# Kernel optimization log

Measured on AMD Instinct MI355X. Metric: run time of the kernel, lower is better.

Reference implementation:

```python
import jax, jax.numpy as jnp
import numpy as np

ALPHA = 0.2          # LeakyReLU negative slope
NEG_BIG = -9e15      # mask fill value from the original code
N, IN_F, OUT_F = 8192, 128, 64


def setup_inputs() -> dict:
    key = jax.random.key(0)
    k1, k2, k3, k4 = jax.random.split(key, 4)
    h = jax.random.normal(k1, (N, IN_F), dtype=jnp.float32)
    adj = jax.random.randint(k2, (N, N), 0, 2, dtype=jnp.int32)
    W = jax.random.normal(k3, (IN_F, OUT_F), dtype=jnp.float32) * 0.1
    a = jax.random.normal(k4, (2 * OUT_F, 1), dtype=jnp.float32) * 0.1
    return {"h": h, "adj": adj, "W": W, "a": a}


def reference(h, adj, W, a):
    # Wh: [N, F]
    Wh = h @ W
    # e_ij = leakyrelu([Wh_i ; Wh_j] . a) = leakyrelu(Wh_i.a1 + Wh_j.a2)
    # (identical math to the original NxNx2F concat, without materializing it)
    a1 = a[:OUT_F, 0]   # [F]
    a2 = a[OUT_F:, 0]   # [F]
    s1 = Wh @ a1        # [N]
    s2 = Wh @ a2        # [N]
    e = jax.nn.leaky_relu(s1[:, None] + s2[None, :], negative_slope=ALPHA)  # [N, N]
    e = jnp.where(adj > 0, e, jnp.float32(NEG_BIG))
    attention = jax.nn.softmax(e, axis=1)
    # dropout is identity at inference (training=False)
    h_prime = attention @ Wh  # [N, F]
    return jax.nn.elu(h_prime)  # concat=True -> elu
```

## Files before the change

### kernel.cpp

```cpp
#include <hip/hip_runtime.h>
#include <hip/hip_bf16.h>

#define N 8192
#define IN_F 128
#define OUT_F 64
#define LRELU_ALPHA 0.2f
#define PAD 520

typedef __attribute__((ext_vector_type(8))) short short8;
typedef __attribute__((ext_vector_type(4))) float float4v;
typedef __attribute__((ext_vector_type(4))) unsigned short ushortx4;

__device__ __forceinline__ unsigned short bf16_bits(float x) {
  unsigned u = __builtin_bit_cast(unsigned, x);
  u += 0x7fffu + ((u >> 16) & 1u);
  return (unsigned short)(u >> 16);
}

__global__ __launch_bounds__(256) void prep_kernel(
    const float* __restrict__ h, const float* __restrict__ W,
    const float* __restrict__ a, float* __restrict__ s1,
    float* __restrict__ s2, unsigned short* __restrict__ whT) {
  const int tid = threadIdx.x;
  const int row = blockIdx.x * 4 + (tid >> 6);
  const int k = tid & 63;
  const float4* hr4 = (const float4*)(h + row * IN_F);
  float acc = 0.f;
#pragma unroll
  for (int c4 = 0; c4 < IN_F / 4; ++c4) {
    const float4 hv = hr4[c4];
    const int cb = c4 * 4;
    acc = fmaf(hv.x, W[(cb + 0) * OUT_F + k], acc);
    acc = fmaf(hv.y, W[(cb + 1) * OUT_F + k], acc);
    acc = fmaf(hv.z, W[(cb + 2) * OUT_F + k], acc);
    acc = fmaf(hv.w, W[(cb + 3) * OUT_F + k], acc);
  }
  whT[(long)k * N + row] = bf16_bits(acc);
  float p1 = acc * a[k];
  float p2 = acc * a[OUT_F + k];
#pragma unroll
  for (int off = 32; off > 0; off >>= 1) {
    p1 += __shfl_xor(p1, off);
    p2 += __shfl_xor(p2, off);
  }
  if (k == 0) { s1[row] = p1; s2[row] = p2; }
}

__global__ __launch_bounds__(256) void repack_kernel(
    const unsigned short* __restrict__ whT, unsigned short* __restrict__ whF) {
  const int f = blockIdx.x * 256 + threadIdx.x;
  const int lane = f & 63, tt = (f >> 6) & 3, c = f >> 8;
  const int r16 = lane & 15, quad = lane >> 4;
  const short8 v = *(const short8*)(whT + (long)(tt * 16 + r16) * N + c * 32 + quad * 8);
  *(short8*)(whF + (long)f * 8) = v;
}

__device__ __forceinline__ void p_write(unsigned short* pr, int c, int4 av,
                                        float4 s2v, float s1w) {
  float e0 = s1w + s2v.x; e0 = fmaxf(e0, LRELU_ALPHA * e0);
  float e1 = s1w + s2v.y; e1 = fmaxf(e1, LRELU_ALPHA * e1);
  float e2 = s1w + s2v.z; e2 = fmaxf(e2, LRELU_ALPHA * e2);
  float e3 = s1w + s2v.w; e3 = fmaxf(e3, LRELU_ALPHA * e3);
  const float p0 = av.x > 0 ? __expf(e0) : 0.f;
  const float p1 = av.y > 0 ? __expf(e1) : 0.f;
  const float p2 = av.z > 0 ? __expf(e2) : 0.f;
  const float p3 = av.w > 0 ? __expf(e3) : 0.f;
  ushortx4 pk = {bf16_bits(p0), bf16_bits(p1), bf16_bits(p2), bf16_bits(p3)};
  *(ushortx4*)(pr + c) = pk;
}

__global__ __launch_bounds__(512, 4) void gat_kernel(
    const int* __restrict__ adj, const float* __restrict__ s1,
    const float* __restrict__ s2, const unsigned short* __restrict__ whF,
    float* __restrict__ out) {
  __shared__ __align__(16) unsigned short pbuf[2][16][PAD];
  const int tid = threadIdx.x;
  const int w = tid >> 6, L = tid & 63;
  const int r16 = L & 15, quad = L >> 4;
  const int row0 = blockIdx.x * 16;
  const int rA = 2 * w, rB = 2 * w + 1;
  const long arowA = (long)(row0 + rA) * N;
  const long arowB = (long)(row0 + rB) * N;
  const float s1A = s1[row0 + rA];
  const float s1B = s1[row0 + rB];
  const int c = L * 4;

  float4v acc0 = {0.f, 0.f, 0.f, 0.f};
  float4v acc1 = {0.f, 0.f, 0.f, 0.f};
  float4v acc2 = {0.f, 0.f, 0.f, 0.f};
  float4v acc3 = {0.f, 0.f, 0.f, 0.f};
  float4v accD = {0.f, 0.f, 0.f, 0.f};
  const short ONE = (short)0x3F80;
  const short8 ones = {ONE, ONE, ONE, ONE, ONE, ONE, ONE, ONE};

  int4 pA0[2], pA1[2], pB0[2], pB1[2];
  float4 ps0, ps1;

  {
    const int4 a0 = *(const int4*)(adj + arowA + c);
    const int4 a1 = *(const int4*)(adj + arowA + 256 + c);
    const int4 b0 = *(const int4*)(adj + arowB + c);
    const int4 b1 = *(const int4*)(adj + arowB + 256 + c);
    const float4 sv0 = *(const float4*)(s2 + c);
    const float4 sv1 = *(const float4*)(s2 + 256 + c);
    pA0[0] = *(const int4*)(adj + arowA + 512 + c);
    pA1[0] = *(const int4*)(adj + arowA + 512 + 256 + c);
    pB0[0] = *(const int4*)(adj + arowB + 512 + c);
    pB1[0] = *(const int4*)(adj + arowB + 512 + 256 + c);
    pA0[1] = *(const int4*)(adj + arowA + 1024 + c);
    pA1[1] = *(const int4*)(adj + arowA + 1024 + 256 + c);
    pB0[1] = *(const int4*)(adj + arowB + 1024 + c);
    pB1[1] = *(const int4*)(adj + arowB + 1024 + 256 + c);
    ps0 = *(const float4*)(s2 + 512 + c);
    ps1 = *(const float4*)(s2 + 512 + 256 + c);
    p_write(pbuf[0][rA], c, a0, sv0, s1A);
    p_write(pbuf[0][rA], 256 + c, a1, sv1, s1A);
    p_write(pbuf[0][rB], c, b0, sv0, s1B);
    p_write(pbuf[0][rB], 256 + c, b1, sv1, s1B);
  }
  __syncthreads();

#pragma unroll
  for (int it = 0; it < 16; ++it) {
    const int b = it & 1;
    const int s = it & 1;
#pragma unroll
    for (int half = 0; half < 2; ++half) {
      const int cc = w + half * 8;
      const short8 afrag = *(const short8*)(&pbuf[b][r16][cc * 32 + quad * 8]);
      const unsigned short* bp = whF + ((long)(it * 16 + cc) * 256 + L) * 8;
      const short8 b0 = *(const short8*)(bp);
      const short8 b1 = *(const short8*)(bp + 512);
      const short8 b2 = *(const short8*)(bp + 1024);
      const short8 b3 = *(const short8*)(bp + 1536);
      acc0 = __builtin_amdgcn_mfma_f32_16x16x32_bf16(afrag, b0, acc0, 0, 0, 0);
      acc1 = __builtin_amdgcn_mfma_f32_16x16x32_bf16(afrag, b1, acc1, 0, 0, 0);
      acc2 = __builtin_amdgcn_mfma_f32_16x16x32_bf16(afrag, b2, acc2, 0, 0, 0);
      acc3 = __builtin_amdgcn_mfma_f32_16x16x32_bf16(afrag, b3, acc3, 0, 0, 0);
      accD = __builtin_amdgcn_mfma_f32_16x16x32_bf16(afrag, ones, accD, 0, 0, 0);
    }
    if (it < 15) {
      unsigned short* prA = pbuf[b ^ 1][rA];
      unsigned short* prB = pbuf[b ^ 1][rB];
      p_write(prA, c, pA0[s], ps0, s1A);
      p_write(prA, 256 + c, pA1[s], ps1, s1A);
      p_write(prB, c, pB0[s], ps0, s1B);
      p_write(prB, 256 + c, pB1[s], ps1, s1B);
      if (it < 13) {
        const long base = (long)(it + 3) * 512 + c;
        pA0[s] = *(const int4*)(adj + arowA + base);
        pA1[s] = *(const int4*)(adj + arowA + base + 256);
        pB0[s] = *(const int4*)(adj + arowB + base);
        pB1[s] = *(const int4*)(adj + arowB + base + 256);
      }
      if (it < 14) {
        ps0 = *(const float4*)(s2 + (it + 2) * 512 + c);
        ps1 = *(const float4*)(s2 + (it + 2) * 512 + 256 + c);
      }
    }
    __syncthreads();
  }

  float* M = (float*)pbuf;
  if (w >= 4) {
    float* S = M + (w - 4) * 1040;
#pragma unroll
    for (int reg = 0; reg < 4; ++reg) {
      const int r = quad * 4 + reg;
      S[r * 64 + 0 * 16 + r16] = acc0[reg];
      S[r * 64 + 1 * 16 + r16] = acc1[reg];
      S[r * 64 + 2 * 16 + r16] = acc2[reg];
      S[r * 64 + 3 * 16 + r16] = acc3[reg];
      if (r16 == 0) S[1024 + r] = accD[reg];
    }
  }
  __syncthreads();
  if (w < 4) {
    float* S = M + w * 1040;
#pragma unroll
    for (int reg = 0; reg < 4; ++reg) {
      const int r = quad * 4 + reg;
      S[r * 64 + 0 * 16 + r16] += acc0[reg];
      S[r * 64 + 1 * 16 + r16] += acc1[reg];
      S[r * 64 + 2 * 16 + r16] += acc2[reg];
      S[r * 64 + 3 * 16 + r16] += acc3[reg];
      if (r16 == 0) S[1024 + r] += accD[reg];
    }
  }
  __syncthreads();
#pragma unroll
  for (int part = 0; part < 2; ++part) {
    const int e = part * 512 + tid;
    const int r = e >> 6, k = e & 63;
    float Sv = 0.f, Lv = 0.f;
#pragma unroll
    for (int sl = 0; sl < 4; ++sl) {
      Sv += M[sl * 1040 + r * 64 + k];
      Lv += M[sl * 1040 + 1024 + r];
    }
    const float v = Sv / Lv;
    out[(long)(row0 + r) * OUT_F + k] = v > 0.f ? v : expm1f(v);
  }
}

extern "C" void kernel_launch(void* const* d_in, const int* in_sizes, int n_in,
                              void* d_out, int out_size, void* d_ws, size_t ws_size,
                              hipStream_t stream) {
  const float* h = (const float*)d_in[0];
  const int* adj = (const int*)d_in[1];
  const float* W = (const float*)d_in[2];
  const float* a = (const float*)d_in[3];
  float* out = (float*)d_out;

  float* s1 = (float*)d_ws;
  float* s2 = s1 + N;
  unsigned short* whT = (unsigned short*)(s2 + N);
  unsigned short* whF = whT + (long)OUT_F * N;

  prep_kernel<<<N / 4, 256, 0, stream>>>(h, W, a, s1, s2, whT);
  repack_kernel<<<N * OUT_F / 8 / 256, 256, 0, stream>>>(whT, whF);
  gat_kernel<<<N / 16, 512, 0, stream>>>(adj, s1, s2, whF, out);
}
```

Measured before the change: 394.6 us.

## Fuse Wh projection and MFMA-fragment repack into one prep kernel

Merges the projection prep kernel and the repack kernel into one kernel. Each block now computes a 32-row tile of Wh from an LDS-staged slice of h and writes it directly in the MFMA fragment layout the attention kernel expects. This removes one launch and the whT intermediate round trip through global memory, and gives more register reuse per W load. The cost is extra LDS traffic and a two-stage reduction for s1/s2. The dominant gat kernel is unchanged, so the effect is limited to the small prep portion.

```diff
diff --git a/kernel.cpp b/kernel.cpp
--- a/kernel.cpp
+++ b/kernel.cpp
@@ -6,6 +6,7 @@
 #define OUT_F 64
 #define LRELU_ALPHA 0.2f
 #define PAD 520
+#define HS_STRIDE 129
 
 typedef __attribute__((ext_vector_type(8))) short short8;
 typedef __attribute__((ext_vector_type(4))) float float4v;
@@ -20,39 +21,80 @@
 __global__ __launch_bounds__(256) void prep_kernel(
     const float* __restrict__ h, const float* __restrict__ W,
     const float* __restrict__ a, float* __restrict__ s1,
-    float* __restrict__ s2, unsigned short* __restrict__ whT) {
+    float* __restrict__ s2, unsigned short* __restrict__ whF) {
+  __shared__ float hs[32 * HS_STRIDE];
+  __shared__ float sred[4][4][8][2];
   const int tid = threadIdx.x;
-  const int row = blockIdx.x * 4 + (tid >> 6);
-  const int k = tid & 63;
-  const float4* hr4 = (const float4*)(h + row * IN_F);
-  float acc = 0.f;
-#pragma unroll
-  for (int c4 = 0; c4 < IN_F / 4; ++c4) {
-    const float4 hv = hr4[c4];
-    const int cb = c4 * 4;
-    acc = fmaf(hv.x, W[(cb + 0) * OUT_F + k], acc);
-    acc = fmaf(hv.y, W[(cb + 1) * OUT_F + k], acc);
-    acc = fmaf(hv.z, W[(cb + 2) * OUT_F + k], acc);
-    acc = fmaf(hv.w, W[(cb + 3) * OUT_F + k], acc);
-  }
-  whT[(long)k * N + row] = bf16_bits(acc);
-  float p1 = acc * a[k];
-  float p2 = acc * a[OUT_F + k];
-#pragma unroll
-  for (int off = 32; off > 0; off >>= 1) {
-    p1 += __shfl_xor(p1, off);
-    p2 += __shfl_xor(p2, off);
-  }
-  if (k == 0) { s1[row] = p1; s2[row] = p2; }
-}
-
-__global__ __launch_bounds__(256) void repack_kernel(
-    const unsigned short* __restrict__ whT, unsigned short* __restrict__ whF) {
-  const int f = blockIdx.x * 256 + threadIdx.x;
-  const int lane = f & 63, tt = (f >> 6) & 3, c = f >> 8;
-  const int r16 = lane & 15, quad = lane >> 4;
-  const short8 v = *(const short8*)(whT + (long)(tt * 16 + r16) * N + c * 32 + quad * 8);
-  *(short8*)(whF + (long)f * 8) = v;
+  const int c32 = blockIdx.x;
+  const int w = tid >> 6, L = tid & 63;
+  const int r16 = L & 15, quad = L >> 4;
+  const int d = w * 16 + r16;
+
+  {
+    const int row = tid >> 3;
+    const int col0 = (tid & 7) * 16;
+    const float4* src = (const float4*)(h + (long)(c32 * 32 + row) * IN_F + col0);
+#pragma unroll
+    for (int i = 0; i < 4; ++i) {
+      const float4 v = src[i];
+      float* dst = hs + row * HS_STRIDE + col0 + i * 4;
+      dst[0] = v.x; dst[1] = v.y; dst[2] = v.z; dst[3] = v.w;
+    }
+  }
+  __syncthreads();
+
+  float acc[8] = {0.f, 0.f, 0.f, 0.f, 0.f, 0.f, 0.f, 0.f};
+  const float* hb = hs + (quad * 8) * HS_STRIDE;
+#pragma unroll 4
+  for (int cidx = 0; cidx < IN_F; ++cidx) {
+    const float wv = W[cidx * OUT_F + d];
+#pragma unroll
+    for (int j = 0; j < 8; ++j)
+      acc[j] = fmaf(hb[j * HS_STRIDE + cidx], wv, acc[j]);
+  }
+
+  {
+    ushortx4 lo = {bf16_bits(acc[0]), bf16_bits(acc[1]),
+                   bf16_bits(acc[2]), bf16_bits(acc[3])};
+    ushortx4 hi = {bf16_bits(acc[4]), bf16_bits(acc[5]),
+                   bf16_bits(acc[6]), bf16_bits(acc[7])};
+    unsigned short* dst = whF + ((long)c32 * 256 + w * 64 + L) * 8;
+    *(ushortx4*)(dst) = lo;
+    *(ushortx4*)(dst + 4) = hi;
+  }
+
+  const float a1d = a[d], a2d = a[OUT_F + d];
+  float p1[8], p2[8];
+#pragma unroll
+  for (int j = 0; j < 8; ++j) { p1[j] = acc[j] * a1d; p2[j] = acc[j] * a2d; }
+#pragma unroll
+  for (int off = 1; off < 16; off <<= 1) {
+#pragma unroll
+    for (int j = 0; j < 8; ++j) {
+      p1[j] += __shfl_xor(p1[j], off);
+      p2[j] += __shfl_xor(p2[j], off);
+    }
+  }
+  if (r16 == 0) {
+#pragma unroll
+    for (int j = 0; j < 8; ++j) {
+      sred[w][quad][j][0] = p1[j];
+      sred[w][quad][j][1] = p2[j];
+    }
+  }
+  __syncthreads();
+  if (tid < 32) {
+    const int q = tid >> 3, j = tid & 7;
+    float v1 = 0.f, v2 = 0.f;
+#pragma unroll
+    for (int ww = 0; ww < 4; ++ww) {
+      v1 += sred[ww][q][j][0];
+      v2 += sred[ww][q][j][1];
+    }
+    const int row = c32 * 32 + q * 8 + j;
+    s1[row] = v1;
+    s2[row] = v2;
+  }
 }
 
 __device__ __forceinline__ void p_write(unsigned short* pr, int c, int4 av,
@@ -214,10 +256,8 @@
 
   float* s1 = (float*)d_ws;
   float* s2 = s1 + N;
-  unsigned short* whT = (unsigned short*)(s2 + N);
-  unsigned short* whF = whT + (long)OUT_F * N;
-
-  prep_kernel<<<N / 4, 256, 0, stream>>>(h, W, a, s1, s2, whT);
-  repack_kernel<<<N * OUT_F / 8 / 256, 256, 0, stream>>>(whT, whF);
+  unsigned short* whF = (unsigned short*)(s2 + N);
+
+  prep_kernel<<<N / 32, 256, 0, stream>>>(h, W, a, s1, s2, whF);
   gat_kernel<<<N / 16, 512, 0, stream>>>(adj, s1, s2, whF, out);
 }
```

Result: no change. 387.8 us (-1.7%).
